# Kernel tuning notes

Measured on AMD Instinct MI355X. Metric: run time of the kernel, lower is better.

## Reference

```python
import jax, jax.numpy as jnp
import numpy as np

EPS = 1e-8
WINDOW = 3      # config.router_window_size
TEMP = 1.0      # config.router_temp (> 0, so sqrt(D) fallback unused)
TOP_K = 2       # config.moe_top_k


def _routing_weights(x, prototypes):
    # L2-normalize router input per token (normalize_router_input=True)
    x = x / jnp.clip(jnp.linalg.norm(x, axis=-1, keepdims=True), EPS)
    # 'window' mode: causal moving average of size WINDOW along seq, with the
    # first token replicated WINDOW-1 times on the left (matches F.conv1d with
    # left pad of flat_input[:, :, [0]] and an averaging kernel).
    w = WINDOW
    padded = jnp.concatenate([jnp.repeat(x[:, :1], w - 1, axis=1), x], axis=1)  # [B, S+w-1, D]
    cs = jnp.concatenate(
        [jnp.zeros_like(padded[:, :1]), jnp.cumsum(padded, axis=1)], axis=1
    )  # [B, S+w, D]
    router_input = (cs[:, w:] - cs[:, :-w]) / w  # [B, S, D] moving mean
    # F.linear(router_input, prototypes): logits over experts
    logits = jnp.einsum('bsd,ed->bse', router_input, prototypes)  # [B, S, E]
    # softmax in float32 (F.softmax(..., dtype=torch.float))
    return jax.nn.softmax((logits / TEMP).astype(jnp.float32), axis=-1)


def setup_inputs() -> dict:
    key = jax.random.key(0)
    k1, k2 = jax.random.split(key)
    bs, sq, D, E = 8, 2048, 1024, 64
    x = jax.random.normal(k1, (bs, sq, D), dtype=jnp.float32)
    prototypes = jax.random.normal(k2, (E, D), dtype=jnp.float32) * 0.02
    attn_mask = jnp.ones((bs, sq), dtype=jnp.int32)
    return {"x": x, "prototypes": prototypes, "attn_mask": attn_mask}


def reference(x, prototypes, attn_mask):
    # attn_mask is all ones here; in 'window' mode it only feeds logging stats.
    routing_weights = _routing_weights(x, prototypes)          # [B, S, E]
    weights, modules = jax.lax.top_k(routing_weights, TOP_K)   # [B, S, K]
    weights = weights / weights.sum(axis=-1, keepdims=True)    # renormalize top-k
    return modules, weights
```

## Files before the change

### kernel.cpp

```cpp
#include <hip/hip_runtime.h>
#include <math.h>


#define BB 8
#define SS 2048
#define DD 1024
#define EE 64
#define EPSV 1e-8f

#define FMA4(A, s, P) \
  A.x += (s) * (P).x; A.y += (s) * (P).y; A.z += (s) * (P).z; A.w += (s) * (P).w;

#define SUMSQ4(v) ((v).x * (v).x + (v).y * (v).y + (v).z * (v).z + (v).w * (v).w)

__global__ __launch_bounds__(256) void repack_proto(
    const float* __restrict__ proto, float* __restrict__ ptt) {
  const int gid = blockIdx.x * 256 + threadIdx.x;
  const int d = gid >> 6;
  const int e = gid & 63;
  ptt[gid] = proto[(size_t)e * DD + d];
}

__global__ __launch_bounds__(256, 2) void router_dots(
    const float* __restrict__ x, const float* __restrict__ ptt,
    float* __restrict__ dots) {
  __shared__ float xt[4][2][16][36];
  __shared__ float B0[32][68];
  __shared__ float B1[32][68];
  __shared__ float nq[4][32];

  const int lane = threadIdx.x & 63;
  const int w    = __builtin_amdgcn_readfirstlane(threadIdx.x >> 6);
  const int b    = blockIdx.x >> 6;
  const int s0   = (blockIdx.x & 63) * 32;

  const int toks = lane & 31;
  const int kh   = lane >> 5;
  const int eg   = lane & 7;
  const int tg   = lane >> 3;

  const float* xb = x + ((size_t)b * SS + s0) * DD;
  const int kbase = w * 256;

  float4 acc0[4], acc1[4];
#pragma unroll
  for (int i = 0; i < 4; ++i) {
    acc0[i] = make_float4(0.f, 0.f, 0.f, 0.f);
    acc1[i] = make_float4(0.f, 0.f, 0.f, 0.f);
  }
  float q = 0.0f;

  {
    const float* xs = xb + (size_t)toks * DD + kbase + kh * 8;
    const float4 va = *(const float4*)(xs);
    const float4 vb = *(const float4*)(xs + 4);
    q += SUMSQ4(va) + SUMSQ4(vb);
    float* dstc = &xt[w][0][0][toks];
    dstc[(kh * 8 + 0) * 36] = va.x;
    dstc[(kh * 8 + 1) * 36] = va.y;
    dstc[(kh * 8 + 2) * 36] = va.z;
    dstc[(kh * 8 + 3) * 36] = va.w;
    dstc[(kh * 8 + 4) * 36] = vb.x;
    dstc[(kh * 8 + 5) * 36] = vb.y;
    dstc[(kh * 8 + 6) * 36] = vb.z;
    dstc[(kh * 8 + 7) * 36] = vb.w;
  }

  float4 pp0[4], pp1[4];
#pragma unroll
  for (int r = 0; r < 4; ++r) {
    const float* pr = ptt + (size_t)(kbase + r) * EE + eg * 8;
    pp0[r] = *(const float4*)(pr);
    pp1[r] = *(const float4*)(pr + 4);
  }

  for (int c = 0; c < 16; ++c) {
    const int cur = c & 1;
    float4 na, nb;
    if (c + 1 < 16) {
      const float* xs = xb + (size_t)toks * DD + kbase + (c + 1) * 16 + kh * 8;
      na = *(const float4*)(xs);
      nb = *(const float4*)(xs + 4);
    }
#pragma unroll
    for (int kk = 0; kk < 16; ++kk) {
      const int slot = kk & 3;
      const float4 xf = *(const float4*)(&xt[w][cur][kk][tg * 4]);
      const float4 p0 = pp0[slot];
      const float4 p1 = pp1[slot];
      int kpre = kbase + c * 16 + kk + 4;
      if (kpre > kbase + 255) kpre = kbase + 255;
      const float* pr = ptt + (size_t)kpre * EE + eg * 8;
      pp0[slot] = *(const float4*)(pr);
      pp1[slot] = *(const float4*)(pr + 4);
      FMA4(acc0[0], xf.x, p0) FMA4(acc1[0], xf.x, p1)
      FMA4(acc0[1], xf.y, p0) FMA4(acc1[1], xf.y, p1)
      FMA4(acc0[2], xf.z, p0) FMA4(acc1[2], xf.z, p1)
      FMA4(acc0[3], xf.w, p0) FMA4(acc1[3], xf.w, p1)
    }
    if (c + 1 < 16) {
      q += SUMSQ4(na) + SUMSQ4(nb);
      float* dstc = &xt[w][cur ^ 1][0][toks];
      dstc[(kh * 8 + 0) * 36] = na.x;
      dstc[(kh * 8 + 1) * 36] = na.y;
      dstc[(kh * 8 + 2) * 36] = na.z;
      dstc[(kh * 8 + 3) * 36] = na.w;
      dstc[(kh * 8 + 4) * 36] = nb.x;
      dstc[(kh * 8 + 5) * 36] = nb.y;
      dstc[(kh * 8 + 6) * 36] = nb.z;
      dstc[(kh * 8 + 7) * 36] = nb.w;
    }
  }

  q += __shfl_xor(q, 32);
  if (kh == 0) nq[w][toks] = q;

#define WRB(R)                                                  \
  { _Pragma("unroll") for (int i = 0; i < 4; ++i) {             \
      *(float4*)(&(R)[tg * 4 + i][eg * 8])     = acc0[i];       \
      *(float4*)(&(R)[tg * 4 + i][eg * 8 + 4]) = acc1[i]; } }
#define ADDB(R)                                                 \
  { _Pragma("unroll") for (int i = 0; i < 4; ++i) {             \
      const float4 t0 = *(const float4*)(&(R)[tg * 4 + i][eg * 8]);     \
      const float4 t1 = *(const float4*)(&(R)[tg * 4 + i][eg * 8 + 4]); \
      acc0[i].x += t0.x; acc0[i].y += t0.y;                     \
      acc0[i].z += t0.z; acc0[i].w += t0.w;                     \
      acc1[i].x += t1.x; acc1[i].y += t1.y;                     \
      acc1[i].z += t1.z; acc1[i].w += t1.w; } }

  __syncthreads();
  if (w == 1) WRB(B0)
  if (w == 3) WRB(B1)
  __syncthreads();
  if (w == 0) ADDB(B0)
  if (w == 2) ADDB(B1)
  __syncthreads();
  if (w == 2) WRB(B0)
  __syncthreads();
  if (w == 0) {
    ADDB(B0)
#pragma unroll
    for (int i = 0; i < 4; ++i) {
      const int row = tg * 4 + i;
      const float qs = nq[0][row] + nq[1][row] + nq[2][row] + nq[3][row];
      const float inv = 1.0f / fmaxf(sqrtf(qs), EPSV);
      float4 o0, o1;
      o0.x = acc0[i].x * inv; o0.y = acc0[i].y * inv;
      o0.z = acc0[i].z * inv; o0.w = acc0[i].w * inv;
      o1.x = acc1[i].x * inv; o1.y = acc1[i].y * inv;
      o1.z = acc1[i].z * inv; o1.w = acc1[i].w * inv;
      float* dp = dots + ((size_t)b * SS + s0 + row) * EE + eg * 8;
      *(float4*)(dp)     = o0;
      *(float4*)(dp + 4) = o1;
    }
  }
}

#define T2UP(s, ei)                                            \
  if ((s) > v1) { v2 = v1; i2 = i1; v1 = (s); i1 = (ei); }     \
  else if ((s) > v2) { v2 = (s); i2 = (ei); }

__global__ __launch_bounds__(256) void router_top2(
    const float* __restrict__ dots, float* __restrict__ out) {
  const int gtid = blockIdx.x * 256 + threadIdx.x;
  const int tok  = gtid >> 1;
  const int h    = gtid & 1;
  const int b    = tok >> 11;
  const int sl   = tok & (SS - 1);
  const int r0   = (sl >= 2) ? sl - 2 : 0;
  const int r1   = (sl >= 1) ? sl - 1 : 0;

  const float* d0 = dots + ((size_t)b * SS + r0) * EE + h * 32;
  const float* d1 = dots + ((size_t)b * SS + r1) * EE + h * 32;
  const float* d2 = dots + ((size_t)b * SS + sl) * EE + h * 32;

  float v1 = -INFINITY, v2 = -INFINITY;
  int i1 = 0, i2 = 0;
#pragma unroll
  for (int qd = 0; qd < 8; ++qd) {
    const float4 a = *(const float4*)(d0 + qd * 4);
    const float4 c = *(const float4*)(d1 + qd * 4);
    const float4 e = *(const float4*)(d2 + qd * 4);
    const int e0 = h * 32 + qd * 4;
    float s;
    s = a.x + c.x + e.x; T2UP(s, e0 + 0)
    s = a.y + c.y + e.y; T2UP(s, e0 + 1)
    s = a.z + c.z + e.z; T2UP(s, e0 + 2)
    s = a.w + c.w + e.w; T2UP(s, e0 + 3)
  }

  {
    const float ov1 = __shfl_xor(v1, 1);
    const int   oi1 = __shfl_xor(i1, 1);
    const float ov2 = __shfl_xor(v2, 1);
    const int   oi2 = __shfl_xor(i2, 1);
    const bool o_beats = (ov1 > v1) || (ov1 == v1 && oi1 < i1);
    if (o_beats) {
      const bool v1_beats_o2 = (v1 > ov2) || (v1 == ov2 && i1 < oi2);
      v2 = v1_beats_o2 ? v1 : ov2;
      i2 = v1_beats_o2 ? i1 : oi2;
      v1 = ov1;
      i1 = oi1;
    } else {
      const bool o1_beats_v2 = (ov1 > v2) || (ov1 == v2 && oi1 < i2);
      if (o1_beats_v2) { v2 = ov1; i2 = oi1; }
    }
  }

  if (h == 0) {
    const float ex = expf((v2 - v1) * (1.0f / 3.0f));
    const float w1 = 1.0f / (1.0f + ex);
    const size_t o = (size_t)tok * 2;
    *(float2*)(out + o) = make_float2((float)i1, (float)i2);
    *(float2*)(out + (size_t)BB * SS * 2 + o) = make_float2(w1, ex * w1);
  }
}

extern "C" void kernel_launch(void* const* d_in, const int* in_sizes, int n_in,
                              void* d_out, int out_size, void* d_ws, size_t ws_size,
                              hipStream_t stream) {
  const float* x     = (const float*)d_in[0];
  const float* proto = (const float*)d_in[1];
  float* out  = (float*)d_out;
  float* ptt  = (float*)d_ws;
  float* dots = (float*)((char*)d_ws + (512 << 10));

  repack_proto<<<dim3(256), dim3(256), 0, stream>>>(proto, ptt);
  router_dots<<<dim3(512), dim3(256), 0, stream>>>(x, ptt, dots);
  router_top2<<<dim3(128), dim3(256), 0, stream>>>(dots, out);
}
```

Measured before the change: 134.4 us.

## Restructure router GEMM to 1024-thread blocks with per-lane token and 16-way K split

Each block now covers 64 tokens with 16 waves, each wave handling a 64-wide K slice. Each lane owns one token and all 64 experts, reading prototype rows as wave-uniform broadcast loads instead of per-lane prefetched registers. The cross-wave partial sums are combined by a multi-stage shared-memory tree reduction with many barriers. The goal is to reuse the broadcast prototype loads across the block and put more threads in flight. The cost is 64 accumulator registers per lane, a long serialized reduction, and only 256 blocks in the grid.

```diff
diff --git a/kernel.cpp b/kernel.cpp
--- a/kernel.cpp
+++ b/kernel.cpp
@@ -7,9 +7,6 @@
 #define DD 1024
 #define EE 64
 #define EPSV 1e-8f
-
-#define FMA4(A, s, P) \
-  A.x += (s) * (P).x; A.y += (s) * (P).y; A.z += (s) * (P).z; A.w += (s) * (P).w;
 
 #define SUMSQ4(v) ((v).x * (v).x + (v).y * (v).y + (v).z * (v).z + (v).w * (v).w)
 
@@ -21,137 +18,153 @@
   ptt[gid] = proto[(size_t)e * DD + d];
 }
 
-__global__ __launch_bounds__(256, 2) void router_dots(
+__global__ __launch_bounds__(1024, 4) void router_dots(
     const float* __restrict__ x, const float* __restrict__ ptt,
     float* __restrict__ dots) {
-  __shared__ float xt[4][2][16][36];
-  __shared__ float B0[32][68];
-  __shared__ float B1[32][68];
-  __shared__ float nq[4][32];
+  __shared__ float SMEM[17408];
 
   const int lane = threadIdx.x & 63;
   const int w    = __builtin_amdgcn_readfirstlane(threadIdx.x >> 6);
-  const int b    = blockIdx.x >> 6;
-  const int s0   = (blockIdx.x & 63) * 32;
+  const int b    = blockIdx.x >> 5;
+  const int s0   = (blockIdx.x & 31) * 64;
 
   const int toks = lane & 31;
   const int kh   = lane >> 5;
-  const int eg   = lane & 7;
-  const int tg   = lane >> 3;
+
+  float* xtw = SMEM + w * 1024;
+  float* nqp = SMEM + 16384;
 
   const float* xb = x + ((size_t)b * SS + s0) * DD;
-  const int kbase = w * 256;
-
-  float4 acc0[4], acc1[4];
-#pragma unroll
-  for (int i = 0; i < 4; ++i) {
-    acc0[i] = make_float4(0.f, 0.f, 0.f, 0.f);
-    acc1[i] = make_float4(0.f, 0.f, 0.f, 0.f);
-  }
-  float q = 0.0f;
+  const int kbase = w * 64;
+
+  float4 acc[16];
+#pragma unroll
+  for (int i = 0; i < 16; ++i) acc[i] = make_float4(0.f, 0.f, 0.f, 0.f);
+  float qA = 0.0f, qB = 0.0f;
 
   {
-    const float* xs = xb + (size_t)toks * DD + kbase + kh * 8;
-    const float4 va = *(const float4*)(xs);
-    const float4 vb = *(const float4*)(xs + 4);
-    q += SUMSQ4(va) + SUMSQ4(vb);
-    float* dstc = &xt[w][0][0][toks];
-    dstc[(kh * 8 + 0) * 36] = va.x;
-    dstc[(kh * 8 + 1) * 36] = va.y;
-    dstc[(kh * 8 + 2) * 36] = va.z;
-    dstc[(kh * 8 + 3) * 36] = va.w;
-    dstc[(kh * 8 + 4) * 36] = vb.x;
-    dstc[(kh * 8 + 5) * 36] = vb.y;
-    dstc[(kh * 8 + 6) * 36] = vb.z;
-    dstc[(kh * 8 + 7) * 36] = vb.w;
-  }
-
-  float4 pp0[4], pp1[4];
-#pragma unroll
-  for (int r = 0; r < 4; ++r) {
-    const float* pr = ptt + (size_t)(kbase + r) * EE + eg * 8;
-    pp0[r] = *(const float4*)(pr);
-    pp1[r] = *(const float4*)(pr + 4);
-  }
-
-  for (int c = 0; c < 16; ++c) {
-    const int cur = c & 1;
-    float4 na, nb;
-    if (c + 1 < 16) {
-      const float* xs = xb + (size_t)toks * DD + kbase + (c + 1) * 16 + kh * 8;
-      na = *(const float4*)(xs);
-      nb = *(const float4*)(xs + 4);
-    }
+    const float* xsA = xb + (size_t)toks * DD + kbase + kh * 8;
+    const float* xsB = xsA + (size_t)32 * DD;
+    const float4 a0 = *(const float4*)(xsA);
+    const float4 a1 = *(const float4*)(xsA + 4);
+    const float4 c0 = *(const float4*)(xsB);
+    const float4 c1 = *(const float4*)(xsB + 4);
+    qA += SUMSQ4(a0) + SUMSQ4(a1);
+    qB += SUMSQ4(c0) + SUMSQ4(c1);
+    float* d0 = xtw + toks;
+    float* d1 = xtw + 32 + toks;
+    d0[(kh * 8 + 0) * 64] = a0.x; d0[(kh * 8 + 1) * 64] = a0.y;
+    d0[(kh * 8 + 2) * 64] = a0.z; d0[(kh * 8 + 3) * 64] = a0.w;
+    d0[(kh * 8 + 4) * 64] = a1.x; d0[(kh * 8 + 5) * 64] = a1.y;
+    d0[(kh * 8 + 6) * 64] = a1.z; d0[(kh * 8 + 7) * 64] = a1.w;
+    d1[(kh * 8 + 0) * 64] = c0.x; d1[(kh * 8 + 1) * 64] = c0.y;
+    d1[(kh * 8 + 2) * 64] = c0.z; d1[(kh * 8 + 3) * 64] = c0.w;
+    d1[(kh * 8 + 4) * 64] = c1.x; d1[(kh * 8 + 5) * 64] = c1.y;
+    d1[(kh * 8 + 6) * 64] = c1.z; d1[(kh * 8 + 7) * 64] = c1.w;
+  }
+
+  for (int c = 0; c < 4; ++c) {
+    float4 a0, a1, c0, c1;
+    if (c + 1 < 4) {
+      const float* xsA = xb + (size_t)toks * DD + kbase + (c + 1) * 16 + kh * 8;
+      const float* xsB = xsA + (size_t)32 * DD;
+      a0 = *(const float4*)(xsA);
+      a1 = *(const float4*)(xsA + 4);
+      c0 = *(const float4*)(xsB);
+      c1 = *(const float4*)(xsB + 4);
+    }
+    const float* pb = ptt + (size_t)(kbase + c * 16) * EE;
 #pragma unroll
     for (int kk = 0; kk < 16; ++kk) {
-      const int slot = kk & 3;
-      const float4 xf = *(const float4*)(&xt[w][cur][kk][tg * 4]);
-      const float4 p0 = pp0[slot];
-      const float4 p1 = pp1[slot];
-      int kpre = kbase + c * 16 + kk + 4;
-      if (kpre > kbase + 255) kpre = kbase + 255;
-      const float* pr = ptt + (size_t)kpre * EE + eg * 8;
-      pp0[slot] = *(const float4*)(pr);
-      pp1[slot] = *(const float4*)(pr + 4);
-      FMA4(acc0[0], xf.x, p0) FMA4(acc1[0], xf.x, p1)
-      FMA4(acc0[1], xf.y, p0) FMA4(acc1[1], xf.y, p1)
-      FMA4(acc0[2], xf.z, p0) FMA4(acc1[2], xf.z, p1)
-      FMA4(acc0[3], xf.w, p0) FMA4(acc1[3], xf.w, p1)
-    }
-    if (c + 1 < 16) {
-      q += SUMSQ4(na) + SUMSQ4(nb);
-      float* dstc = &xt[w][cur ^ 1][0][toks];
-      dstc[(kh * 8 + 0) * 36] = na.x;
-      dstc[(kh * 8 + 1) * 36] = na.y;
-      dstc[(kh * 8 + 2) * 36] = na.z;
-      dstc[(kh * 8 + 3) * 36] = na.w;
-      dstc[(kh * 8 + 4) * 36] = nb.x;
-      dstc[(kh * 8 + 5) * 36] = nb.y;
-      dstc[(kh * 8 + 6) * 36] = nb.z;
-      dstc[(kh * 8 + 7) * 36] = nb.w;
-    }
-  }
-
-  q += __shfl_xor(q, 32);
-  if (kh == 0) nq[w][toks] = q;
-
-#define WRB(R)                                                  \
-  { _Pragma("unroll") for (int i = 0; i < 4; ++i) {             \
-      *(float4*)(&(R)[tg * 4 + i][eg * 8])     = acc0[i];       \
-      *(float4*)(&(R)[tg * 4 + i][eg * 8 + 4]) = acc1[i]; } }
-#define ADDB(R)                                                 \
-  { _Pragma("unroll") for (int i = 0; i < 4; ++i) {             \
-      const float4 t0 = *(const float4*)(&(R)[tg * 4 + i][eg * 8]);     \
-      const float4 t1 = *(const float4*)(&(R)[tg * 4 + i][eg * 8 + 4]); \
-      acc0[i].x += t0.x; acc0[i].y += t0.y;                     \
-      acc0[i].z += t0.z; acc0[i].w += t0.w;                     \
-      acc1[i].x += t1.x; acc1[i].y += t1.y;                     \
-      acc1[i].z += t1.z; acc1[i].w += t1.w; } }
-
-  __syncthreads();
-  if (w == 1) WRB(B0)
-  if (w == 3) WRB(B1)
-  __syncthreads();
-  if (w == 0) ADDB(B0)
-  if (w == 2) ADDB(B1)
-  __syncthreads();
-  if (w == 2) WRB(B0)
+      const float xk = xtw[kk * 64 + lane];
+      const float4* pk = (const float4*)(pb + kk * EE);
+#pragma unroll
+      for (int i = 0; i < 16; ++i) {
+        const float4 pv = pk[i];
+        acc[i].x += xk * pv.x;
+        acc[i].y += xk * pv.y;
+        acc[i].z += xk * pv.z;
+        acc[i].w += xk * pv.w;
+      }
+    }
+    if (c + 1 < 4) {
+      qA += SUMSQ4(a0) + SUMSQ4(a1);
+      qB += SUMSQ4(c0) + SUMSQ4(c1);
+      float* d0 = xtw + toks;
+      float* d1 = xtw + 32 + toks;
+      d0[(kh * 8 + 0) * 64] = a0.x; d0[(kh * 8 + 1) * 64] = a0.y;
+      d0[(kh * 8 + 2) * 64] = a0.z; d0[(kh * 8 + 3) * 64] = a0.w;
+      d0[(kh * 8 + 4) * 64] = a1.x; d0[(kh * 8 + 5) * 64] = a1.y;
+      d0[(kh * 8 + 6) * 64] = a1.z; d0[(kh * 8 + 7) * 64] = a1.w;
+      d1[(kh * 8 + 0) * 64] = c0.x; d1[(kh * 8 + 1) * 64] = c0.y;
+      d1[(kh * 8 + 2) * 64] = c0.z; d1[(kh * 8 + 3) * 64] = c0.w;
+      d1[(kh * 8 + 4) * 64] = c1.x; d1[(kh * 8 + 5) * 64] = c1.y;
+      d1[(kh * 8 + 6) * 64] = c1.z; d1[(kh * 8 + 7) * 64] = c1.w;
+    }
+  }
+
+  qA += __shfl_xor(qA, 32);
+  qB += __shfl_xor(qB, 32);
+  if (kh == 0) {
+    nqp[w * 64 + toks]      = qA;
+    nqp[w * 64 + 32 + toks] = qB;
+  }
+
+  float* B0 = SMEM;
+  float* B1 = SMEM + 4864;
+
+#define WRB(R)                                                       \
+  { _Pragma("unroll") for (int i = 0; i < 16; ++i)                   \
+      *(float4*)((R) + lane * 76 + i * 4) = acc[i]; }
+#define ADDB(R)                                                      \
+  { _Pragma("unroll") for (int i = 0; i < 16; ++i) {                 \
+      const float4 t = *(const float4*)((R) + lane * 76 + i * 4);    \
+      acc[i].x += t.x; acc[i].y += t.y;                              \
+      acc[i].z += t.z; acc[i].w += t.w; } }
+
+  __syncthreads();
+  if (w == 1) WRB(B0)  if (w == 5) WRB(B1)
+  __syncthreads();
+  if (w == 0) ADDB(B0) if (w == 4) ADDB(B1)
+  __syncthreads();
+  if (w == 3) WRB(B0)  if (w == 7) WRB(B1)
+  __syncthreads();
+  if (w == 2) ADDB(B0) if (w == 6) ADDB(B1)
+  __syncthreads();
+  if (w == 9) WRB(B0)  if (w == 13) WRB(B1)
+  __syncthreads();
+  if (w == 8) ADDB(B0) if (w == 12) ADDB(B1)
+  __syncthreads();
+  if (w == 11) WRB(B0) if (w == 15) WRB(B1)
+  __syncthreads();
+  if (w == 10) ADDB(B0) if (w == 14) ADDB(B1)
+  __syncthreads();
+  if (w == 2) WRB(B0)  if (w == 6) WRB(B1)
+  __syncthreads();
+  if (w == 0) ADDB(B0) if (w == 4) ADDB(B1)
+  __syncthreads();
+  if (w == 10) WRB(B0) if (w == 14) WRB(B1)
+  __syncthreads();
+  if (w == 8) ADDB(B0) if (w == 12) ADDB(B1)
+  __syncthreads();
+  if (w == 4) WRB(B0)  if (w == 12) WRB(B1)
+  __syncthreads();
+  if (w == 0) ADDB(B0) if (w == 8) ADDB(B1)
+  __syncthreads();
+  if (w == 8) WRB(B0)
   __syncthreads();
   if (w == 0) {
     ADDB(B0)
-#pragma unroll
-    for (int i = 0; i < 4; ++i) {
-      const int row = tg * 4 + i;
-      const float qs = nq[0][row] + nq[1][row] + nq[2][row] + nq[3][row];
-      const float inv = 1.0f / fmaxf(sqrtf(qs), EPSV);
-      float4 o0, o1;
-      o0.x = acc0[i].x * inv; o0.y = acc0[i].y * inv;
-      o0.z = acc0[i].z * inv; o0.w = acc0[i].w * inv;
-      o1.x = acc1[i].x * inv; o1.y = acc1[i].y * inv;
-      o1.z = acc1[i].z * inv; o1.w = acc1[i].w * inv;
-      float* dp = dots + ((size_t)b * SS + s0 + row) * EE + eg * 8;
-      *(float4*)(dp)     = o0;
-      *(float4*)(dp + 4) = o1;
+    float qs = 0.0f;
+#pragma unroll
+    for (int i = 0; i < 16; ++i) qs += nqp[i * 64 + lane];
+    const float inv = 1.0f / fmaxf(sqrtf(qs), EPSV);
+    float* dp = dots + ((size_t)b * SS + s0 + lane) * EE;
+#pragma unroll
+    for (int i = 0; i < 16; ++i) {
+      float4 o = acc[i];
+      o.x *= inv; o.y *= inv; o.z *= inv; o.w *= inv;
+      *(float4*)(dp + i * 4) = o;
     }
   }
 }
@@ -226,6 +239,6 @@
   float* dots = (float*)((char*)d_ws + (512 << 10));
 
   repack_proto<<<dim3(256), dim3(256), 0, stream>>>(proto, ptt);
-  router_dots<<<dim3(512), dim3(256), 0, stream>>>(x, ptt, dots);
+  router_dots<<<dim3(256), dim3(1024), 0, stream>>>(x, ptt, dots);
   router_top2<<<dim3(128), dim3(256), 0, stream>>>(dots, out);
 }
```

Measured after the change: 207.6 us. +54.5%, slower.

## Retile router dot kernel to 1024-thread blocks with 64 tokens per block

Applied to the files above, without the earlier changes.

Restructures the router GEMM so each 1024-thread block handles 64 tokens: four wave groups split the 64 experts and four split K, and each lane owns one token with 16 experts. Prototype values become wave-uniform loads (the same address for all lanes, read straight from memory without prefetching). The token tile is shared in LDS across the expert groups and synchronised with a block barrier every chunk. The aim is to halve the grid, reuse each x tile across expert groups, and cut redundant x traffic. The cost is a per-chunk __syncthreads, lower per-thread ILP from one token per lane, and only 256 blocks, which may underfill the GPU.

```diff
diff --git a/kernel.cpp b/kernel.cpp
--- a/kernel.cpp
+++ b/kernel.cpp
@@ -7,11 +7,6 @@
 #define DD 1024
 #define EE 64
 #define EPSV 1e-8f
-
-#define FMA4(A, s, P) \
-  A.x += (s) * (P).x; A.y += (s) * (P).y; A.z += (s) * (P).z; A.w += (s) * (P).w;
-
-#define SUMSQ4(v) ((v).x * (v).x + (v).y * (v).y + (v).z * (v).z + (v).w * (v).w)
 
 __global__ __launch_bounds__(256) void repack_proto(
     const float* __restrict__ proto, float* __restrict__ ptt) {
@@ -21,138 +16,124 @@
   ptt[gid] = proto[(size_t)e * DD + d];
 }
 
-__global__ __launch_bounds__(256, 2) void router_dots(
+__global__ __launch_bounds__(1024) void router_dots(
     const float* __restrict__ x, const float* __restrict__ ptt,
     float* __restrict__ dots) {
-  __shared__ float xt[4][2][16][36];
-  __shared__ float B0[32][68];
-  __shared__ float B1[32][68];
-  __shared__ float nq[4][32];
-
-  const int lane = threadIdx.x & 63;
-  const int w    = __builtin_amdgcn_readfirstlane(threadIdx.x >> 6);
-  const int b    = blockIdx.x >> 6;
-  const int s0   = (blockIdx.x & 63) * 32;
-
-  const int toks = lane & 31;
-  const int kh   = lane >> 5;
-  const int eg   = lane & 7;
-  const int tg   = lane >> 3;
-
-  const float* xb = x + ((size_t)b * SS + s0) * DD;
-  const int kbase = w * 256;
-
-  float4 acc0[4], acc1[4];
-#pragma unroll
-  for (int i = 0; i < 4; ++i) {
-    acc0[i] = make_float4(0.f, 0.f, 0.f, 0.f);
-    acc1[i] = make_float4(0.f, 0.f, 0.f, 0.f);
-  }
+  __shared__ float SMEM[8448];
+
+  const int tid  = threadIdx.x;
+  const int lane = tid & 63;
+  const int w    = __builtin_amdgcn_readfirstlane(tid >> 6);
+  const int we   = w & 3;
+  const int wk   = w >> 2;
+  const int b    = blockIdx.x >> 5;
+  const int s0   = (blockIdx.x & 31) * 64;
+
+  const int gl = tid & 255;
+  const int st = gl >> 2;
+  const int sq = gl & 3;
+
+  float* xtw = SMEM + wk * 2048;
+  float* nqp = SMEM + 8192;
+
+  const float* xsrow =
+      x + ((size_t)b * SS + s0 + st) * DD + wk * 256 + sq * 4;
+  const float* pr = ptt + (size_t)(wk * 256) * EE + we * 16;
+
+  float4 acc0 = make_float4(0.f, 0.f, 0.f, 0.f);
+  float4 acc1 = make_float4(0.f, 0.f, 0.f, 0.f);
+  float4 acc2 = make_float4(0.f, 0.f, 0.f, 0.f);
+  float4 acc3 = make_float4(0.f, 0.f, 0.f, 0.f);
   float q = 0.0f;
 
   {
-    const float* xs = xb + (size_t)toks * DD + kbase + kh * 8;
-    const float4 va = *(const float4*)(xs);
-    const float4 vb = *(const float4*)(xs + 4);
-    q += SUMSQ4(va) + SUMSQ4(vb);
-    float* dstc = &xt[w][0][0][toks];
-    dstc[(kh * 8 + 0) * 36] = va.x;
-    dstc[(kh * 8 + 1) * 36] = va.y;
-    dstc[(kh * 8 + 2) * 36] = va.z;
-    dstc[(kh * 8 + 3) * 36] = va.w;
-    dstc[(kh * 8 + 4) * 36] = vb.x;
-    dstc[(kh * 8 + 5) * 36] = vb.y;
-    dstc[(kh * 8 + 6) * 36] = vb.z;
-    dstc[(kh * 8 + 7) * 36] = vb.w;
-  }
-
-  float4 pp0[4], pp1[4];
-#pragma unroll
-  for (int r = 0; r < 4; ++r) {
-    const float* pr = ptt + (size_t)(kbase + r) * EE + eg * 8;
-    pp0[r] = *(const float4*)(pr);
-    pp1[r] = *(const float4*)(pr + 4);
-  }
+    const float4 v = *(const float4*)(xsrow);
+    float* d = xtw + (sq * 4) * 64 + st;
+    d[0]   = v.x;
+    d[64]  = v.y;
+    d[128] = v.z;
+    d[192] = v.w;
+  }
+  __syncthreads();
 
   for (int c = 0; c < 16; ++c) {
-    const int cur = c & 1;
-    float4 na, nb;
-    if (c + 1 < 16) {
-      const float* xs = xb + (size_t)toks * DD + kbase + (c + 1) * 16 + kh * 8;
-      na = *(const float4*)(xs);
-      nb = *(const float4*)(xs + 4);
-    }
+    const int buf = c & 1;
+    float4 nv;
+    if (c + 1 < 16) nv = *(const float4*)(xsrow + (c + 1) * 16);
+    const float* xk_base = xtw + buf * 1024 + lane;
+    const float* pp = pr + (size_t)(c * 16) * EE;
 #pragma unroll
     for (int kk = 0; kk < 16; ++kk) {
-      const int slot = kk & 3;
-      const float4 xf = *(const float4*)(&xt[w][cur][kk][tg * 4]);
-      const float4 p0 = pp0[slot];
-      const float4 p1 = pp1[slot];
-      int kpre = kbase + c * 16 + kk + 4;
-      if (kpre > kbase + 255) kpre = kbase + 255;
-      const float* pr = ptt + (size_t)kpre * EE + eg * 8;
-      pp0[slot] = *(const float4*)(pr);
-      pp1[slot] = *(const float4*)(pr + 4);
-      FMA4(acc0[0], xf.x, p0) FMA4(acc1[0], xf.x, p1)
-      FMA4(acc0[1], xf.y, p0) FMA4(acc1[1], xf.y, p1)
-      FMA4(acc0[2], xf.z, p0) FMA4(acc1[2], xf.z, p1)
-      FMA4(acc0[3], xf.w, p0) FMA4(acc1[3], xf.w, p1)
+      const float xk = xk_base[kk * 64];
+      q += xk * xk;
+      const float4 p0 = *(const float4*)(pp + kk * 64);
+      const float4 p1 = *(const float4*)(pp + kk * 64 + 4);
+      const float4 p2 = *(const float4*)(pp + kk * 64 + 8);
+      const float4 p3 = *(const float4*)(pp + kk * 64 + 12);
+      acc0.x += xk * p0.x; acc0.y += xk * p0.y;
+      acc0.z += xk * p0.z; acc0.w += xk * p0.w;
+      acc1.x += xk * p1.x; acc1.y += xk * p1.y;
+      acc1.z += xk * p1.z; acc1.w += xk * p1.w;
+      acc2.x += xk * p2.x; acc2.y += xk * p2.y;
+      acc2.z += xk * p2.z; acc2.w += xk * p2.w;
+      acc3.x += xk * p3.x; acc3.y += xk * p3.y;
+      acc3.z += xk * p3.z; acc3.w += xk * p3.w;
     }
     if (c + 1 < 16) {
-      q += SUMSQ4(na) + SUMSQ4(nb);
-      float* dstc = &xt[w][cur ^ 1][0][toks];
-      dstc[(kh * 8 + 0) * 36] = na.x;
-      dstc[(kh * 8 + 1) * 36] = na.y;
-      dstc[(kh * 8 + 2) * 36] = na.z;
-      dstc[(kh * 8 + 3) * 36] = na.w;
-      dstc[(kh * 8 + 4) * 36] = nb.x;
-      dstc[(kh * 8 + 5) * 36] = nb.y;
-      dstc[(kh * 8 + 6) * 36] = nb.z;
-      dstc[(kh * 8 + 7) * 36] = nb.w;
+      float* d = xtw + (buf ^ 1) * 1024 + (sq * 4) * 64 + st;
+      d[0]   = nv.x;
+      d[64]  = nv.y;
+      d[128] = nv.z;
+      d[192] = nv.w;
     }
-  }
-
-  q += __shfl_xor(q, 32);
-  if (kh == 0) nq[w][toks] = q;
-
-#define WRB(R)                                                  \
-  { _Pragma("unroll") for (int i = 0; i < 4; ++i) {             \
-      *(float4*)(&(R)[tg * 4 + i][eg * 8])     = acc0[i];       \
-      *(float4*)(&(R)[tg * 4 + i][eg * 8 + 4]) = acc1[i]; } }
-#define ADDB(R)                                                 \
-  { _Pragma("unroll") for (int i = 0; i < 4; ++i) {             \
-      const float4 t0 = *(const float4*)(&(R)[tg * 4 + i][eg * 8]);     \
-      const float4 t1 = *(const float4*)(&(R)[tg * 4 + i][eg * 8 + 4]); \
-      acc0[i].x += t0.x; acc0[i].y += t0.y;                     \
-      acc0[i].z += t0.z; acc0[i].w += t0.w;                     \
-      acc1[i].x += t1.x; acc1[i].y += t1.y;                     \
-      acc1[i].z += t1.z; acc1[i].w += t1.w; } }
-
-  __syncthreads();
-  if (w == 1) WRB(B0)
-  if (w == 3) WRB(B1)
-  __syncthreads();
-  if (w == 0) ADDB(B0)
-  if (w == 2) ADDB(B1)
-  __syncthreads();
-  if (w == 2) WRB(B0)
-  __syncthreads();
-  if (w == 0) {
+    __syncthreads();
+  }
+
+  if (we == 0) nqp[wk * 64 + lane] = q;
+
+  float* B0 = SMEM;
+  float* B1 = SMEM + 4096;
+
+#define WRB(R)                                              \
+  { float* p_ = (R) + we * 1024 + lane * 4;                 \
+    *(float4*)(p_ + 0)   = acc0;                            \
+    *(float4*)(p_ + 256) = acc1;                            \
+    *(float4*)(p_ + 512) = acc2;                            \
+    *(float4*)(p_ + 768) = acc3; }
+#define ADDB(R)                                             \
+  { const float* p_ = (R) + we * 1024 + lane * 4;           \
+    const float4 t0 = *(const float4*)(p_ + 0);             \
+    const float4 t1 = *(const float4*)(p_ + 256);           \
+    const float4 t2 = *(const float4*)(p_ + 512);           \
+    const float4 t3 = *(const float4*)(p_ + 768);           \
+    acc0.x += t0.x; acc0.y += t0.y; acc0.z += t0.z; acc0.w += t0.w; \
+    acc1.x += t1.x; acc1.y += t1.y; acc1.z += t1.z; acc1.w += t1.w; \
+    acc2.x += t2.x; acc2.y += t2.y; acc2.z += t2.z; acc2.w += t2.w; \
+    acc3.x += t3.x; acc3.y += t3.y; acc3.z += t3.z; acc3.w += t3.w; }
+
+  __syncthreads();
+  if (wk == 1) WRB(B0)
+  if (wk == 3) WRB(B1)
+  __syncthreads();
+  if (wk == 0) ADDB(B0)
+  if (wk == 2) ADDB(B1)
+  __syncthreads();
+  if (wk == 2) WRB(B0)
+  __syncthreads();
+  if (wk == 0) {
     ADDB(B0)
-#pragma unroll
-    for (int i = 0; i < 4; ++i) {
-      const int row = tg * 4 + i;
-      const float qs = nq[0][row] + nq[1][row] + nq[2][row] + nq[3][row];
-      const float inv = 1.0f / fmaxf(sqrtf(qs), EPSV);
-      float4 o0, o1;
-      o0.x = acc0[i].x * inv; o0.y = acc0[i].y * inv;
-      o0.z = acc0[i].z * inv; o0.w = acc0[i].w * inv;
-      o1.x = acc1[i].x * inv; o1.y = acc1[i].y * inv;
-      o1.z = acc1[i].z * inv; o1.w = acc1[i].w * inv;
-      float* dp = dots + ((size_t)b * SS + s0 + row) * EE + eg * 8;
-      *(float4*)(dp)     = o0;
-      *(float4*)(dp + 4) = o1;
-    }
+    const float qs = nqp[lane] + nqp[64 + lane] +
+                     nqp[128 + lane] + nqp[192 + lane];
+    const float inv = 1.0f / fmaxf(sqrtf(qs), EPSV);
+    acc0.x *= inv; acc0.y *= inv; acc0.z *= inv; acc0.w *= inv;
+    acc1.x *= inv; acc1.y *= inv; acc1.z *= inv; acc1.w *= inv;
+    acc2.x *= inv; acc2.y *= inv; acc2.z *= inv; acc2.w *= inv;
+    acc3.x *= inv; acc3.y *= inv; acc3.z *= inv; acc3.w *= inv;
+    float* dp = dots + ((size_t)b * SS + s0 + lane) * EE + we * 16;
+    *(float4*)(dp)      = acc0;
+    *(float4*)(dp + 4)  = acc1;
+    *(float4*)(dp + 8)  = acc2;
+    *(float4*)(dp + 12) = acc3;
   }
 }
 
@@ -226,6 +207,6 @@
   float* dots = (float*)((char*)d_ws + (512 << 10));
 
   repack_proto<<<dim3(256), dim3(256), 0, stream>>>(proto, ptt);
-  router_dots<<<dim3(512), dim3(256), 0, stream>>>(x, ptt, dots);
+  router_dots<<<dim3(256), dim3(1024), 0, stream>>>(x, ptt, dots);
   router_top2<<<dim3(128), dim3(256), 0, stream>>>(dots, out);
 }
```

Result: no change. 132.5 us (-1.4%).
